# Optimization experiments

Measured on AMD Instinct MI355X. Metric: run time of the kernel, lower is better.

The kernel has to match this reference:

```python
import jax, jax.numpy as jnp
import numpy as np

B, C, H, W = 8, 256, 64, 64
HEADS = 8
DH = C // HEADS          # dim_head = in_ch // heads (as constructed in BasicTransBlock)
RS = 16                  # reduce_size
EPS = 1e-5               # BatchNorm eps


def _rel_pos_index():
    # Swin-style relative position index over the RS x RS reduced grid
    coords = np.stack(np.meshgrid(np.arange(RS), np.arange(RS), indexing='ij')).reshape(2, -1)
    rel = coords[:, :, None] - coords[:, None, :]
    rel = rel.transpose(1, 2, 0).copy()
    rel[:, :, 0] += RS - 1
    rel[:, :, 1] += RS - 1
    rel[:, :, 0] *= 2 * RS - 1
    return jnp.asarray(rel.sum(-1))  # [RS*RS, RS*RS] int

REL_IDX = _rel_pos_index()


def setup_inputs() -> dict:
    key = jax.random.key(0)
    ks = jax.random.split(key, 8)
    f32 = jnp.float32
    return {
        "x": jax.random.normal(ks[0], (B, C, H, W), f32),
        "bn1_gamma": jnp.ones((C,), f32),
        "bn1_beta": jnp.zeros((C,), f32),
        "bn1_mean": jnp.zeros((C,), f32),
        "bn1_var": jnp.ones((C,), f32),
        "qkv_dw": jax.random.normal(ks[1], (C, 1, 3, 3), f32) * 0.05,   # depthwise 3x3
        "qkv_pw": jax.random.normal(ks[2], (3 * C, C), f32) * 0.05,     # pointwise 1x1 -> 3C
        "out_dw": jax.random.normal(ks[3], (C, 1, 3, 3), f32) * 0.05,
        "out_pw": jax.random.normal(ks[4], (C, C), f32) * 0.05,
        "rel_table": jax.random.normal(ks[5], ((2 * RS - 1) ** 2, HEADS), f32) * 0.02,
        "bn2_gamma": jnp.ones((C,), f32),
        "bn2_beta": jnp.zeros((C,), f32),
        "bn2_mean": jnp.zeros((C,), f32),
        "bn2_var": jnp.ones((C,), f32),
        "mlp_w": jax.random.normal(ks[6], (C, C), f32) * 0.05,          # 1x1 conv, no bias
    }


def _bn(x, gamma, beta, mean, var):
    # inference-mode BatchNorm2d
    inv = gamma * jax.lax.rsqrt(var + EPS)
    return x * inv[None, :, None, None] + (beta - mean * inv)[None, :, None, None]


def _dwconv3(x, w):
    # depthwise 3x3, stride 1, padding 1
    return jax.lax.conv_general_dilated(
        x, w, (1, 1), 'SAME', feature_group_count=x.shape[1],
        dimension_numbers=('NCHW', 'OIHW', 'NCHW'))


def _interp_ac(x, oh, ow):
    # bilinear resize, align_corners=True (matches F.interpolate(..., align_corners=True))
    _, _, h, w = x.shape
    ys = jnp.linspace(0.0, h - 1.0, oh)
    xs = jnp.linspace(0.0, w - 1.0, ow)
    y0 = jnp.floor(ys).astype(jnp.int32); y1 = jnp.minimum(y0 + 1, h - 1)
    x0 = jnp.floor(xs).astype(jnp.int32); x1 = jnp.minimum(x0 + 1, w - 1)
    wy = (ys - y0.astype(ys.dtype))[:, None]   # [oh,1]
    wx = (xs - x0.astype(xs.dtype))            # [ow]
    v = x[:, :, y0, :] * (1 - wy) + x[:, :, y1, :] * wy      # [B,C,oh,w]
    return v[:, :, :, x0] * (1 - wx) + v[:, :, :, x1] * wx   # [B,C,oh,ow]


def _split_heads(t, h, w):
    # channel layout in rearrange is (dim_head heads): c = d*HEADS + head
    b = t.shape[0]
    return t.reshape(b, DH, HEADS, h * w).transpose(0, 2, 3, 1)  # [B,heads,hw,DH]


def _rel_bias(rel_table):
    bias = rel_table[REL_IDX.reshape(-1)].reshape(RS, RS, RS * RS, HEADS)
    bias = jnp.repeat(bias, H // RS, axis=0)   # expand rows to H
    bias = jnp.repeat(bias, W // RS, axis=1)   # expand cols to W
    return bias.reshape(H * W, RS * RS, HEADS).transpose(2, 0, 1)  # [heads, HW, RS*RS]


def reference(x, bn1_gamma, bn1_beta, bn1_mean, bn1_var,
              qkv_dw, qkv_pw, out_dw, out_pw, rel_table,
              bn2_gamma, bn2_beta, bn2_mean, bn2_var, mlp_w):
    out = _bn(x, bn1_gamma, bn1_beta, bn1_mean, bn1_var)

    # --- LinearAttention ---
    qkv = jnp.einsum('bchw,oc->bohw', _dwconv3(out, qkv_dw), qkv_pw)
    q, k, v = jnp.split(qkv, 3, axis=1)
    k = _interp_ac(k, RS, RS)
    v = _interp_ac(v, RS, RS)
    q = _split_heads(q, H, W)       # [B,heads,HW,DH]
    k = _split_heads(k, RS, RS)     # [B,heads,RS^2,DH]
    v = _split_heads(v, RS, RS)
    attn = jnp.einsum('bhid,bhjd->bhij', q, k)
    attn = (attn + _rel_bias(rel_table)[None]) * (DH ** -0.5)  # bias added BEFORE scale, as in source
    attn = jax.nn.softmax(attn, axis=-1)
    o = jnp.einsum('bhij,bhjd->bhid', attn, v)                 # [B,heads,HW,DH]
    o = o.transpose(0, 3, 1, 2).reshape(x.shape[0], C, H, W)   # inverse of (dim_head heads) split
    o = jnp.einsum('bchw,oc->bohw', _dwconv3(o, out_dw), out_pw)

    out = o + x
    residue = out
    out = jax.nn.relu(_bn(out, bn2_gamma, bn2_beta, bn2_mean, bn2_var))
    out = jnp.einsum('bchw,oc->bohw', out, mlp_w)
    return out + residue
```

## Files before the change

### kernel.cpp

```cpp
#include <hip/hip_runtime.h>
#include <hip/hip_bf16.h>
#include <math.h>

#define EPSF 1e-5f

typedef float f32x4 __attribute__((ext_vector_type(4)));
typedef short short8 __attribute__((ext_vector_type(8)));
typedef short short4v __attribute__((ext_vector_type(4)));
typedef unsigned short u16x4 __attribute__((ext_vector_type(4)));
typedef unsigned short u16x8 __attribute__((ext_vector_type(8)));

#if defined(__has_builtin)
#if __has_builtin(__builtin_amdgcn_mfma_f32_16x16x16bf16_1k)
#define HAVE_MFMA16 1
#endif
#endif
#ifndef HAVE_MFMA16
#define HAVE_MFMA16 0
#endif

static __device__ __forceinline__ unsigned short f2bf(float f) {
    unsigned u = __float_as_uint(f);
    u = (u + 0x7FFF + ((u >> 16) & 1)) >> 16;
    return (unsigned short)u;
}

static __device__ __forceinline__ float bf2f(unsigned short u) {
    return __uint_as_float((unsigned)u << 16);
}

static __device__ __forceinline__ unsigned packbf2(float a, float b) {
    __hip_bfloat162 t = __float22bfloat162_rn(float2{a, b});
    union { __hip_bfloat162 v; unsigned u; } cv;
    cv.v = t;
    return cv.u;
}

static __device__ __forceinline__ float fexp2(float x) {
    return __builtin_amdgcn_exp2f(x);
}

static __device__ __forceinline__ void lgkm_barrier() {
    asm volatile("s_waitcnt lgkmcnt(0)\n\ts_barrier" ::: "memory");
    __builtin_amdgcn_sched_barrier(0);
}

static __device__ __forceinline__ int swz(int r) { return ((r ^ (r >> 2)) & 7) << 1; }

#define ATTN_SCALE 0.17677669529663687f
#define LOG2E      1.4426950408889634f
#define QSCALE     (ATTN_SCALE * LOG2E)

template<bool BN, bool IB, bool OBF>
__global__ __launch_bounds__(256) void dwconv_k(
    const void* __restrict__ X, const float* __restrict__ DW,
    const float* __restrict__ g, const float* __restrict__ be,
    const float* __restrict__ mn, const float* __restrict__ vr,
    void* __restrict__ Out)
{
    int tid = threadIdx.x;
    int plane = blockIdx.x * 2 + (tid >> 7);
    int c = plane & 255;
    float inv = 1.f, ad = 0.f;
    if (BN) {
        inv = g[c] * rsqrtf(vr[c] + EPSF);
        ad  = be[c] - mn[c] * inv;
    }
    float w[9];
#pragma unroll
    for (int i = 0; i < 9; ++i) w[i] = DW[c * 9 + i];
    const float* Xf          = (const float*)X + (size_t)plane * 4096;
    const unsigned short* Xh = (const unsigned short*)X + (size_t)plane * 4096;
    int u  = tid & 127;
    int y0 = (u >> 3) * 4;
    int x0 = (u & 7) * 8;

    float r[6][16];
#pragma unroll
    for (int rr = 0; rr < 6; ++rr) {
        int yy = y0 + rr - 1;
        bool rv = (unsigned)yy < 64u;
#pragma unroll
        for (int gq = 0; gq < 4; ++gq) {
            int xx = x0 - 4 + gq * 4;
            f32x4 v = {0.f, 0.f, 0.f, 0.f};
            if (rv && (unsigned)xx < 64u) {
                if (IB) {
                    u16x4 u4 = *(const u16x4*)&Xh[yy * 64 + xx];
                    v[0] = bf2f(u4[0]); v[1] = bf2f(u4[1]);
                    v[2] = bf2f(u4[2]); v[3] = bf2f(u4[3]);
                } else {
                    v = *(const f32x4*)&Xf[yy * 64 + xx];
                }
                if (BN) {
#pragma unroll
                    for (int j = 0; j < 4; ++j) v[j] = v[j] * inv + ad;
                }
            }
            r[rr][gq * 4 + 0] = v[0]; r[rr][gq * 4 + 1] = v[1];
            r[rr][gq * 4 + 2] = v[2]; r[rr][gq * 4 + 3] = v[3];
        }
    }

#pragma unroll
    for (int j = 0; j < 4; ++j) {
        float acc[8] = {};
#pragma unroll
        for (int ky = 0; ky < 3; ++ky) {
#pragma unroll
            for (int kx = 0; kx < 3; ++kx) {
                float ww = w[ky * 3 + kx];
#pragma unroll
                for (int p = 0; p < 8; ++p)
                    acc[p] += ww * r[j + ky][3 + p + kx];
            }
        }
        if (OBF) {
            unsigned short* Ob = (unsigned short*)Out + (size_t)plane * 4096;
            int4 pk = { (int)packbf2(acc[0], acc[1]), (int)packbf2(acc[2], acc[3]),
                        (int)packbf2(acc[4], acc[5]), (int)packbf2(acc[6], acc[7]) };
            *(int4*)&Ob[(y0 + j) * 64 + x0] = pk;
        } else {
            float* Ob = (float*)Out + (size_t)plane * 4096;
            f32x4 lo = {acc[0], acc[1], acc[2], acc[3]};
            f32x4 hi = {acc[4], acc[5], acc[6], acc[7]};
            *(f32x4*)&Ob[(y0 + j) * 64 + x0]     = lo;
            *(f32x4*)&Ob[(y0 + j) * 64 + x0 + 4] = hi;
        }
    }
}

__global__ __launch_bounds__(256) void interp_k(
    const unsigned short* __restrict__ T, float* __restrict__ R)
{
    int bc = blockIdx.x;
    const unsigned short* Tb = T + (size_t)bc * 4096;
    int p  = threadIdx.x;
    int oy = p >> 4, ox = p & 15;
    const float st = 63.0f / 15.0f;
    float fy = oy * st, fx = ox * st;
    int y0 = (int)floorf(fy); int y1 = min(y0 + 1, 63); float wy = fy - (float)y0;
    int x0 = (int)floorf(fx); int x1 = min(x0 + 1, 63); float wx = fx - (float)x0;
    float v00 = bf2f(Tb[y0 * 64 + x0]), v01 = bf2f(Tb[y0 * 64 + x1]);
    float v10 = bf2f(Tb[y1 * 64 + x0]), v11 = bf2f(Tb[y1 * 64 + x1]);
    R[(size_t)bc * 256 + p] =
        (1.f - wy) * ((1.f - wx) * v00 + wx * v01) +
        wy         * ((1.f - wx) * v10 + wx * v11);
}

__global__ __launch_bounds__(256) void bias_k(
    const float* __restrict__ rel, float* __restrict__ btab)
{
    int idx = blockIdx.x * 256 + threadIdx.x;
    int h   = idx >> 16;
    int qc  = (idx >> 8) & 255;
    int key = idx & 255;
    int ay = qc >> 4, ax = qc & 15, by = key >> 4, bx = key & 15;
    int t = (ay - by + 15) * 31 + (ax - bx + 15);
    btab[idx] = rel[t * 8 + h] * QSCALE;
}

__global__ __launch_bounds__(256) void kvt_k(
    const unsigned short* __restrict__ kv,
    unsigned short* __restrict__ khat, unsigned short* __restrict__ vhat)
{
    __shared__ unsigned short kt_[32 * 260];
    int bh = blockIdx.x;
    int b = bh >> 3, h = bh & 7;
    const unsigned short* kvb = kv + (size_t)b * 512 * 256;
    int tid = threadIdx.x;

#pragma unroll
    for (int it = 0; it < 8; ++it) {
        int idx = it * 256 + tid;
        int d = idx >> 6, k4 = (idx & 63) * 4;
        ushort4 v = *(const ushort4*)&kvb[(size_t)(256 + d * 8 + h) * 256 + k4];
        *(ushort4*)&vhat[(size_t)bh * 8192 + d * 256 + k4] = v;
    }
#pragma unroll
    for (int it = 0; it < 8; ++it) {
        int idx = it * 256 + tid;
        int d = idx >> 6, k4 = (idx & 63) * 4;
        ushort4 v = *(const ushort4*)&kvb[(size_t)(d * 8 + h) * 256 + k4];
        *(ushort4*)&kt_[d * 260 + k4] = v;
    }
    __syncthreads();
#pragma unroll
    for (int it = 0; it < 8; ++it) {
        int idx = it * 256 + tid;
        int key = idx >> 3, dq = idx & 7;
        ushort4 o;
        o.x = kt_[(dq * 4 + 0) * 260 + key];
        o.y = kt_[(dq * 4 + 1) * 260 + key];
        o.z = kt_[(dq * 4 + 2) * 260 + key];
        o.w = kt_[(dq * 4 + 3) * 260 + key];
        *(ushort4*)&khat[(size_t)bh * 8192 + key * 32 + dq * 4] = o;
    }
}

template<int MODE, bool OB, bool AB, bool QHAT, bool XB>
__global__ __launch_bounds__(256) void mgemm_k(
    const void* __restrict__ A, const float* __restrict__ W,
    float* __restrict__ Out, const void* __restrict__ X,
    const float* __restrict__ g, const float* __restrict__ be,
    const float* __restrict__ mn, const float* __restrict__ vr,
    int M, int Ntot)
{
    __shared__ short Ws[128 * 256];
    __shared__ short As[128 * 64];
    int b = blockIdx.z, m0 = blockIdx.x * 128, n0 = blockIdx.y * 128;
    int tid = threadIdx.x;
    const float* Abf          = (const float*)A + (size_t)b * 256 * M;
    const unsigned short* Abh = (const unsigned short*)A + (size_t)b * 256 * M;

#pragma unroll
    for (int it = 0; it < 32; ++it) {
        int idx = it * 256 + tid;
        int n = idx >> 6, kq = idx & 63;
        f32x4 w4 = *(const f32x4*)&W[(size_t)(n0 + n) * 256 + kq * 4];
        short4v pk = { (short)f2bf(w4[0]), (short)f2bf(w4[1]),
                       (short)f2bf(w4[2]), (short)f2bf(w4[3]) };
        *(short4v*)&Ws[n * 256 + ((kq ^ swz(n)) << 2)] = pk;
    }

    constexpr bool RAW16 = AB && (MODE != 2);
    int mg = tid & 31, kg = tid >> 5;
    f32x4 rg[8];
    u16x4 rg16[8];
    auto load_tile = [&](int k0) {
#pragma unroll
        for (int half = 0; half < 2; ++half) {
#pragma unroll
            for (int i = 0; i < 4; ++i) {
                int c = k0 + kg * 4 + half * 32 + i;
                if (RAW16) {
                    rg16[half * 4 + i] = *(const u16x4*)&Abh[(size_t)c * M + m0 + mg * 4];
                } else if (AB) {
                    u16x4 r4 = *(const u16x4*)&Abh[(size_t)c * M + m0 + mg * 4];
                    float iv = g[c] * rsqrtf(vr[c] + EPSF);
                    float ad = be[c] - mn[c] * iv;
                    f32x4 v;
#pragma unroll
                    for (int j = 0; j < 4; ++j)
                        v[j] = fmaxf(bf2f(r4[j]) * iv + ad, 0.f);
                    rg[half * 4 + i] = v;
                } else {
                    f32x4 v = *(const f32x4*)&Abf[(size_t)c * M + m0 + mg * 4];
                    if (MODE == 2) {
                        float iv = g[c] * rsqrtf(vr[c] + EPSF);
                        float ad = be[c] - mn[c] * iv;
#pragma unroll
                        for (int j = 0; j < 4; ++j) v[j] = fmaxf(v[j] * iv + ad, 0.f);
                    }
                    rg[half * 4 + i] = v;
                }
            }
        }
    };
    load_tile(0);

    int w = tid >> 6, lane = tid & 63;
    int wm = w & 1, wn = w >> 1;
    int lg = lane >> 4, lc = lane & 15;
    f32x4 acc[4][4] = {};

    for (int k0 = 0; k0 < 256; k0 += 64) {
        __syncthreads();
#pragma unroll
        for (int half = 0; half < 2; ++half) {
#pragma unroll
            for (int j = 0; j < 4; ++j) {
                int m = mg * 4 + j;
                short4v pk;
                if (RAW16) {
                    pk = short4v{ (short)rg16[half * 4 + 0][j], (short)rg16[half * 4 + 1][j],
                                  (short)rg16[half * 4 + 2][j], (short)rg16[half * 4 + 3][j] };
                } else {
                    pk = short4v{ (short)f2bf(rg[half * 4 + 0][j]), (short)f2bf(rg[half * 4 + 1][j]),
                                  (short)f2bf(rg[half * 4 + 2][j]), (short)f2bf(rg[half * 4 + 3][j]) };
                }
                *(short4v*)&As[m * 64 + (((kg + half * 8) ^ swz(m)) << 2)] = pk;
            }
        }
        __syncthreads();
        if (k0 < 192) load_tile(k0 + 64);
#pragma unroll
        for (int ksl = 0; ksl < 2; ++ksl) {
            short8 wf[4], af[4];
            int gk = (k0 + ksl * 32 + lg * 8) >> 2;
            int ga = (ksl * 32 + lg * 8) >> 2;
#pragma unroll
            for (int nt = 0; nt < 4; ++nt) {
                int n = wn * 64 + nt * 16 + lc;
                wf[nt] = *(const short8*)&Ws[n * 256 + ((gk ^ swz(n)) << 2)];
            }
#pragma unroll
            for (int mt = 0; mt < 4; ++mt) {
                int m = wm * 64 + mt * 16 + lc;
                af[mt] = *(const short8*)&As[m * 64 + ((ga ^ swz(m)) << 2)];
            }
#pragma unroll
            for (int nt = 0; nt < 4; ++nt)
#pragma unroll
                for (int mt = 0; mt < 4; ++mt)
                    acc[nt][mt] = __builtin_amdgcn_mfma_f32_16x16x32_bf16(
                        wf[nt], af[mt], acc[nt][mt], 0, 0, 0);
        }
    }

    if (QHAT) {
        __syncthreads();
        unsigned short* Os = (unsigned short*)Ws;
#pragma unroll
        for (int nt = 0; nt < 4; ++nt)
#pragma unroll
            for (int mt = 0; mt < 4; ++mt)
#pragma unroll
                for (int reg = 0; reg < 4; ++reg) {
                    int nl = wn * 64 + nt * 16 + lg * 4 + reg;
                    int ml = wm * 64 + mt * 16 + lc;
                    Os[nl * 130 + ml] = f2bf(acc[nt][mt][reg] * QSCALE);
                }
        __syncthreads();
        unsigned short* Oq = (unsigned short*)Out;
        int dbase = n0 >> 3;
#pragma unroll
        for (int it = 0; it < 4; ++it) {
            int ri = it * 256 + tid;
            int hh = ri >> 7, ml = ri & 127;
            u16x8 lo, hi;
#pragma unroll
            for (int dd = 0; dd < 8; ++dd) {
                lo[dd] = Os[(dd * 8 + hh) * 130 + ml];
                hi[dd] = Os[((dd + 8) * 8 + hh) * 130 + ml];
            }
            size_t base = ((size_t)(b * 8 + hh) * 4096 + m0 + ml) * 32 + dbase;
            *(u16x8*)&Oq[base]     = lo;
            *(u16x8*)&Oq[base + 8] = hi;
        }
        return;
    }

    size_t ob = (size_t)b * Ntot * M;
#pragma unroll
    for (int nt = 0; nt < 4; ++nt) {
#pragma unroll
        for (int mt = 0; mt < 4; ++mt) {
#pragma unroll
            for (int reg = 0; reg < 4; ++reg) {
                int n = n0 + wn * 64 + nt * 16 + lg * 4 + reg;
                int m = m0 + wm * 64 + mt * 16 + lc;
                size_t addr = ob + (size_t)n * M + m;
                float v = acc[nt][mt][reg];
                if (MODE >= 1) {
                    float xv = XB ? bf2f(((const unsigned short*)X)[addr])
                                  : ((const float*)X)[addr];
                    v += xv;
                }
                if (OB) ((unsigned short*)Out)[addr] = f2bf(v);
                else    Out[addr] = v;
            }
        }
    }
}

__global__ __launch_bounds__(256) void attn_mfma_k(
    const unsigned short* __restrict__ Qh, const unsigned short* __restrict__ Khat,
    const unsigned short* __restrict__ Vhat,
    const float* __restrict__ btab, unsigned short* __restrict__ O)
{
    __shared__ float Om[2][4][16][36];
    __shared__ float Lw[2][4][16];

    int b = blockIdx.z, h = blockIdx.y, chunk = blockIdx.x;
    int tid = threadIdx.x;
    int w = tid >> 6, lane = tid & 63;
    int lg = lane >> 4, lc = lane & 15;
    int kw = w * 64;

    const unsigned short* Kb = Khat + (size_t)(b * 8 + h) * 8192;
    const unsigned short* Vb = Vhat + (size_t)(b * 8 + h) * 8192;
    const unsigned short* Qb = Qh + (size_t)(b * 8 + h) * 131072;
    unsigned short* Ob = O + (size_t)b * 256 * 4096;
    const float* bt = btab + (size_t)h * 65536;
    int rw = chunk * 128;

    int mrow = tid & 15, md = tid >> 4;

    short8 kf[4];
#pragma unroll
    for (int kt = 0; kt < 4; ++kt)
        kf[kt] = *(const short8*)&Kb[(kw + kt * 16 + lc) * 32 + lg * 8];

#if HAVE_MFMA16
    short4v vq[4][2];
#pragma unroll
    for (int kt = 0; kt < 4; ++kt) {
#pragma unroll
        for (int half = 0; half < 2; ++half)
            vq[kt][half] = *(const short4v*)&Vb[(half * 16 + lc) * 256 + kw + kt * 16 + lg * 4];
    }
#else
    int s1 = ((lg & 1) << 5) + lc;
    int s2 = s1 + 16;
    bool useOdd = (lg >> 1) != 0;
    short8 vf0[2], vf1[2];
#pragma unroll
    for (int ks = 0; ks < 2; ++ks) {
        vf0[ks] = *(const short8*)&Vb[lc * 256 + kw + ks * 32 + lg * 8];
        vf1[ks] = *(const short8*)&Vb[(16 + lc) * 256 + kw + ks * 32 + lg * 8];
    }
#endif

    auto compute = [&](int mt, int buf) {
        int rbase = rw + mt * 16;
        int r_a = rbase + lc;
        int qc = ((r_a >> 8) << 4) | ((r_a >> 2) & 15);
        const float* bq = bt + (size_t)qc * 256 + kw + lg * 4;

        f32x4 sacc[4];
#pragma unroll
        for (int kt = 0; kt < 4; ++kt)
            sacc[kt] = *(const f32x4*)&bq[kt * 16];

        short8 qf = *(const short8*)&Qb[(size_t)r_a * 32 + lg * 8];

#pragma unroll
        for (int kt = 0; kt < 4; ++kt)
            sacc[kt] = __builtin_amdgcn_mfma_f32_16x16x32_bf16(kf[kt], qf, sacc[kt], 0, 0, 0);

        float ls = 0.f;
        f32x4 o0 = {0.f, 0.f, 0.f, 0.f}, o1 = {0.f, 0.f, 0.f, 0.f};

#if HAVE_MFMA16
#pragma unroll
        for (int kt = 0; kt < 4; ++kt) {
            float p0 = fexp2(sacc[kt][0]);
            float p1 = fexp2(sacc[kt][1]);
            float p2 = fexp2(sacc[kt][2]);
            float p3 = fexp2(sacc[kt][3]);
            ls += (p0 + p1) + (p2 + p3);
            int2 pi = { (int)packbf2(p0, p1), (int)packbf2(p2, p3) };
            short4v pa = *(short4v*)&pi;
            o0 = __builtin_amdgcn_mfma_f32_16x16x16bf16_1k(pa, vq[kt][0], o0, 0, 0, 0);
            o1 = __builtin_amdgcn_mfma_f32_16x16x16bf16_1k(pa, vq[kt][1], o1, 0, 0, 0);
        }
        ls += __shfl_xor(ls, 16);
        ls += __shfl_xor(ls, 32);
#pragma unroll
        for (int reg = 0; reg < 4; ++reg) {
            Om[buf][w][lg * 4 + reg][lc]      = o0[reg];
            Om[buf][w][lg * 4 + reg][16 + lc] = o1[reg];
        }
#else
        unsigned plo[4], phi[4];
#pragma unroll
        for (int kt = 0; kt < 4; ++kt) {
            float p0 = fexp2(sacc[kt][0]);
            float p1 = fexp2(sacc[kt][1]);
            float p2 = fexp2(sacc[kt][2]);
            float p3 = fexp2(sacc[kt][3]);
            ls += (p0 + p1) + (p2 + p3);
            plo[kt] = packbf2(p0, p1);
            phi[kt] = packbf2(p2, p3);
        }
        ls += __shfl_xor(ls, 16);
        ls += __shfl_xor(ls, 32);
#pragma unroll
        for (int ks = 0; ks < 2; ++ks) {
            int eA = __shfl((int)plo[2 * ks], s1), oA = __shfl((int)plo[2 * ks + 1], s1);
            int eB = __shfl((int)phi[2 * ks], s1), oB = __shfl((int)phi[2 * ks + 1], s1);
            int eC = __shfl((int)plo[2 * ks], s2), oC = __shfl((int)plo[2 * ks + 1], s2);
            int eD = __shfl((int)phi[2 * ks], s2), oD = __shfl((int)phi[2 * ks + 1], s2);
            int4 pi = { useOdd ? oA : eA, useOdd ? oB : eB,
                        useOdd ? oC : eC, useOdd ? oD : eD };
            short8 pf = *(short8*)&pi;
            o0 = __builtin_amdgcn_mfma_f32_16x16x32_bf16(vf0[ks], pf, o0, 0, 0, 0);
            o1 = __builtin_amdgcn_mfma_f32_16x16x32_bf16(vf1[ks], pf, o1, 0, 0, 0);
        }
        *(f32x4*)&Om[buf][w][lc][lg * 4]      = o0;
        *(f32x4*)&Om[buf][w][lc][16 + lg * 4] = o1;
#endif
        if (lg == 0) Lw[buf][w][lc] = ls;
    };

    auto merge = [&](int mt, int buf) {
        int rbase = rw + mt * 16;
        float L = Lw[buf][0][mrow] + Lw[buf][1][mrow]
                + Lw[buf][2][mrow] + Lw[buf][3][mrow];
        float inv = __builtin_amdgcn_rcpf(L);
        float a0 = Om[buf][0][mrow][md] + Om[buf][1][mrow][md]
                 + Om[buf][2][mrow][md] + Om[buf][3][mrow][md];
        float a1 = Om[buf][0][mrow][md + 16] + Om[buf][1][mrow][md + 16]
                 + Om[buf][2][mrow][md + 16] + Om[buf][3][mrow][md + 16];
        unsigned pk = packbf2(a0 * inv, a1 * inv);
        Ob[(size_t)(md * 8 + h) * 4096 + rbase + mrow]        = (unsigned short)pk;
        Ob[(size_t)((md + 16) * 8 + h) * 4096 + rbase + mrow] = (unsigned short)(pk >> 16);
    };

    compute(0, 0);
    for (int mt = 0; mt < 8; ++mt) {
        lgkm_barrier();
        if (mt < 7) compute(mt + 1, (mt + 1) & 1);
        merge(mt, mt & 1);
    }
}

extern "C" void kernel_launch(void* const* d_in, const int* in_sizes, int n_in,
                              void* d_out, int out_size, void* d_ws, size_t ws_size,
                              hipStream_t stream)
{
    const float* x       = (const float*)d_in[0];
    const float* bn1_g   = (const float*)d_in[1];
    const float* bn1_b   = (const float*)d_in[2];
    const float* bn1_m   = (const float*)d_in[3];
    const float* bn1_v   = (const float*)d_in[4];
    const float* qkv_dw  = (const float*)d_in[5];
    const float* qkv_pw  = (const float*)d_in[6];
    const float* out_dw  = (const float*)d_in[7];
    const float* out_pw  = (const float*)d_in[8];
    const float* rel     = (const float*)d_in[9];
    const float* bn2_g   = (const float*)d_in[10];
    const float* bn2_b   = (const float*)d_in[11];
    const float* bn2_m   = (const float*)d_in[12];
    const float* bn2_v   = (const float*)d_in[13];
    const float* mlp_w   = (const float*)d_in[14];
    float* out = (float*)d_out;

    float* ws = (float*)d_ws;
    float* t    = ws;
    float* q    = ws + (size_t)8 * 1024 * 1024;
    float* tr   = ws + (size_t)16 * 1024 * 1024;
    float* kv   = tr + 524288;
    float* btab = kv + 524288;
    float* khat = btab + 524288;
    float* vhat = khat + 262144;
    float* o   = t;
    float* t2  = q;
    float* a   = t;

    bias_k<<<dim3(2048), 256, 0, stream>>>(rel, btab);

    dwconv_k<true, false, true><<<dim3(1024), 256, 0, stream>>>(
        x, qkv_dw, bn1_g, bn1_b, bn1_m, bn1_v, t);

    mgemm_k<0, true, true, true, false><<<dim3(32, 2, 8), 256, 0, stream>>>(
        t, qkv_pw, q, nullptr, nullptr, nullptr, nullptr, nullptr,
        4096, 256);

    interp_k<<<dim3(2048), 256, 0, stream>>>((const unsigned short*)t, tr);

    mgemm_k<0, true, false, false, false><<<dim3(2, 4, 8), 256, 0, stream>>>(
        tr, qkv_pw + 256 * 256, kv, nullptr, nullptr, nullptr, nullptr, nullptr,
        256, 512);

    kvt_k<<<dim3(64), 256, 0, stream>>>(
        (const unsigned short*)kv, (unsigned short*)khat, (unsigned short*)vhat);

    attn_mfma_k<<<dim3(32, 8, 8), 256, 0, stream>>>(
        (const unsigned short*)q, (const unsigned short*)khat,
        (const unsigned short*)vhat, btab, (unsigned short*)o);

    dwconv_k<false, true, true><<<dim3(1024), 256, 0, stream>>>(
        o, out_dw, nullptr, nullptr, nullptr, nullptr, t2);

    mgemm_k<1, true, true, false, false><<<dim3(32, 2, 8), 256, 0, stream>>>(
        t2, out_pw, (float*)a, x, nullptr, nullptr, nullptr, nullptr,
        4096, 256);

    mgemm_k<2, false, true, false, true><<<dim3(32, 2, 8), 256, 0, stream>>>(
        a, mlp_w, out, a, bn2_g, bn2_b, bn2_m, bn2_v,
        4096, 256);
}
```

Baseline: 129.3 us.

## Split attention work by query rows per wave instead of by key chunks

Each wave now owns 32 query rows and loops over all 256 keys itself, keeping the running sums in registers. Before, four waves split the keys and merged partial outputs through double-buffered shared memory with block barriers. This drops the cross-wave reduction, the barriers and most of the LDS traffic. In exchange every wave reloads the K/V fragments for each key chunk from global/L2 and holds more accumulator registers.

```diff
diff --git a/kernel.cpp b/kernel.cpp
--- a/kernel.cpp
+++ b/kernel.cpp
@@ -38,11 +38,6 @@
 
 static __device__ __forceinline__ float fexp2(float x) {
     return __builtin_amdgcn_exp2f(x);
-}
-
-static __device__ __forceinline__ void lgkm_barrier() {
-    asm volatile("s_waitcnt lgkmcnt(0)\n\ts_barrier" ::: "memory");
-    __builtin_amdgcn_sched_barrier(0);
 }
 
 static __device__ __forceinline__ int swz(int r) { return ((r ^ (r >> 2)) & 7) << 1; }
@@ -369,140 +364,143 @@
     const unsigned short* __restrict__ Vhat,
     const float* __restrict__ btab, unsigned short* __restrict__ O)
 {
-    __shared__ float Om[2][4][16][36];
-    __shared__ float Lw[2][4][16];
+    __shared__ float Ow[4][16][33];
 
     int b = blockIdx.z, h = blockIdx.y, chunk = blockIdx.x;
     int tid = threadIdx.x;
     int w = tid >> 6, lane = tid & 63;
     int lg = lane >> 4, lc = lane & 15;
-    int kw = w * 64;
 
     const unsigned short* Kb = Khat + (size_t)(b * 8 + h) * 8192;
     const unsigned short* Vb = Vhat + (size_t)(b * 8 + h) * 8192;
     const unsigned short* Qb = Qh + (size_t)(b * 8 + h) * 131072;
     unsigned short* Ob = O + (size_t)b * 256 * 4096;
     const float* bt = btab + (size_t)h * 65536;
-    int rw = chunk * 128;
-
-    int mrow = tid & 15, md = tid >> 4;
-
-    short8 kf[4];
-#pragma unroll
-    for (int kt = 0; kt < 4; ++kt)
-        kf[kt] = *(const short8*)&Kb[(kw + kt * 16 + lc) * 32 + lg * 8];
-
+    int rw = chunk * 128 + w * 32;
+
+    short8 qf[2];
+    int qc[2];
+#pragma unroll
+    for (int t = 0; t < 2; ++t) {
+        int r_a = rw + t * 16 + lc;
+        qf[t] = *(const short8*)&Qb[(size_t)r_a * 32 + lg * 8];
+        qc[t] = ((r_a >> 8) << 4) | ((r_a >> 2) & 15);
+    }
+
+    f32x4 o[2][2] = {};
+    float ls[2] = {0.f, 0.f};
+
+    for (int c = 0; c < 4; ++c) {
+        int kc = c * 64;
+        short8 kf[4];
+#pragma unroll
+        for (int kt = 0; kt < 4; ++kt)
+            kf[kt] = *(const short8*)&Kb[(kc + kt * 16 + lc) * 32 + lg * 8];
 #if HAVE_MFMA16
-    short4v vq[4][2];
-#pragma unroll
-    for (int kt = 0; kt < 4; ++kt) {
-#pragma unroll
-        for (int half = 0; half < 2; ++half)
-            vq[kt][half] = *(const short4v*)&Vb[(half * 16 + lc) * 256 + kw + kt * 16 + lg * 4];
-    }
+        short4v vq[4][2];
+#pragma unroll
+        for (int kt = 0; kt < 4; ++kt) {
+#pragma unroll
+            for (int half = 0; half < 2; ++half)
+                vq[kt][half] = *(const short4v*)&Vb[(half * 16 + lc) * 256 + kc + kt * 16 + lg * 4];
+        }
 #else
-    int s1 = ((lg & 1) << 5) + lc;
-    int s2 = s1 + 16;
-    bool useOdd = (lg >> 1) != 0;
-    short8 vf0[2], vf1[2];
-#pragma unroll
-    for (int ks = 0; ks < 2; ++ks) {
-        vf0[ks] = *(const short8*)&Vb[lc * 256 + kw + ks * 32 + lg * 8];
-        vf1[ks] = *(const short8*)&Vb[(16 + lc) * 256 + kw + ks * 32 + lg * 8];
-    }
-#endif
-
-    auto compute = [&](int mt, int buf) {
-        int rbase = rw + mt * 16;
-        int r_a = rbase + lc;
-        int qc = ((r_a >> 8) << 4) | ((r_a >> 2) & 15);
-        const float* bq = bt + (size_t)qc * 256 + kw + lg * 4;
-
-        f32x4 sacc[4];
-#pragma unroll
-        for (int kt = 0; kt < 4; ++kt)
-            sacc[kt] = *(const f32x4*)&bq[kt * 16];
-
-        short8 qf = *(const short8*)&Qb[(size_t)r_a * 32 + lg * 8];
-
-#pragma unroll
-        for (int kt = 0; kt < 4; ++kt)
-            sacc[kt] = __builtin_amdgcn_mfma_f32_16x16x32_bf16(kf[kt], qf, sacc[kt], 0, 0, 0);
-
-        float ls = 0.f;
-        f32x4 o0 = {0.f, 0.f, 0.f, 0.f}, o1 = {0.f, 0.f, 0.f, 0.f};
+        int s1 = ((lg & 1) << 5) + lc;
+        int s2 = s1 + 16;
+        bool useOdd = (lg >> 1) != 0;
+        short8 vf0[2], vf1[2];
+#pragma unroll
+        for (int ks = 0; ks < 2; ++ks) {
+            vf0[ks] = *(const short8*)&Vb[lc * 256 + kc + ks * 32 + lg * 8];
+            vf1[ks] = *(const short8*)&Vb[(16 + lc) * 256 + kc + ks * 32 + lg * 8];
+        }
+#endif
+
+#pragma unroll
+        for (int t = 0; t < 2; ++t) {
+            const float* bq = bt + (size_t)qc[t] * 256 + kc + lg * 4;
+            f32x4 sacc[4];
+#pragma unroll
+            for (int kt = 0; kt < 4; ++kt)
+                sacc[kt] = *(const f32x4*)&bq[kt * 16];
+#pragma unroll
+            for (int kt = 0; kt < 4; ++kt)
+                sacc[kt] = __builtin_amdgcn_mfma_f32_16x16x32_bf16(kf[kt], qf[t], sacc[kt], 0, 0, 0);
 
 #if HAVE_MFMA16
 #pragma unroll
-        for (int kt = 0; kt < 4; ++kt) {
-            float p0 = fexp2(sacc[kt][0]);
-            float p1 = fexp2(sacc[kt][1]);
-            float p2 = fexp2(sacc[kt][2]);
-            float p3 = fexp2(sacc[kt][3]);
-            ls += (p0 + p1) + (p2 + p3);
-            int2 pi = { (int)packbf2(p0, p1), (int)packbf2(p2, p3) };
-            short4v pa = *(short4v*)&pi;
-            o0 = __builtin_amdgcn_mfma_f32_16x16x16bf16_1k(pa, vq[kt][0], o0, 0, 0, 0);
-            o1 = __builtin_amdgcn_mfma_f32_16x16x16bf16_1k(pa, vq[kt][1], o1, 0, 0, 0);
-        }
-        ls += __shfl_xor(ls, 16);
-        ls += __shfl_xor(ls, 32);
+            for (int kt = 0; kt < 4; ++kt) {
+                float p0 = fexp2(sacc[kt][0]);
+                float p1 = fexp2(sacc[kt][1]);
+                float p2 = fexp2(sacc[kt][2]);
+                float p3 = fexp2(sacc[kt][3]);
+                ls[t] += (p0 + p1) + (p2 + p3);
+                int2 pi = { (int)packbf2(p0, p1), (int)packbf2(p2, p3) };
+                short4v pa = *(short4v*)&pi;
+                o[t][0] = __builtin_amdgcn_mfma_f32_16x16x16bf16_1k(pa, vq[kt][0], o[t][0], 0, 0, 0);
+                o[t][1] = __builtin_amdgcn_mfma_f32_16x16x16bf16_1k(pa, vq[kt][1], o[t][1], 0, 0, 0);
+            }
+#else
+            unsigned plo[4], phi[4];
+#pragma unroll
+            for (int kt = 0; kt < 4; ++kt) {
+                float p0 = fexp2(sacc[kt][0]);
+                float p1 = fexp2(sacc[kt][1]);
+                float p2 = fexp2(sacc[kt][2]);
+                float p3 = fexp2(sacc[kt][3]);
+                ls[t] += (p0 + p1) + (p2 + p3);
+                plo[kt] = packbf2(p0, p1);
+                phi[kt] = packbf2(p2, p3);
+            }
+#pragma unroll
+            for (int ks = 0; ks < 2; ++ks) {
+                int eA = __shfl((int)plo[2 * ks], s1), oA = __shfl((int)plo[2 * ks + 1], s1);
+                int eB = __shfl((int)phi[2 * ks], s1), oB = __shfl((int)phi[2 * ks + 1], s1);
+                int eC = __shfl((int)plo[2 * ks], s2), oC = __shfl((int)plo[2 * ks + 1], s2);
+                int eD = __shfl((int)phi[2 * ks], s2), oD = __shfl((int)phi[2 * ks + 1], s2);
+                int4 pi = { useOdd ? oA : eA, useOdd ? oB : eB,
+                            useOdd ? oC : eC, useOdd ? oD : eD };
+                short8 pf = *(short8*)&pi;
+                o[t][0] = __builtin_amdgcn_mfma_f32_16x16x32_bf16(vf0[ks], pf, o[t][0], 0, 0, 0);
+                o[t][1] = __builtin_amdgcn_mfma_f32_16x16x32_bf16(vf1[ks], pf, o[t][1], 0, 0, 0);
+            }
+#endif
+        }
+    }
+
+#pragma unroll
+    for (int t = 0; t < 2; ++t) {
+        float L = ls[t];
+        L += __shfl_xor(L, 16);
+        L += __shfl_xor(L, 32);
+        float inv = __builtin_amdgcn_rcpf(L);
+#if HAVE_MFMA16
 #pragma unroll
         for (int reg = 0; reg < 4; ++reg) {
-            Om[buf][w][lg * 4 + reg][lc]      = o0[reg];
-            Om[buf][w][lg * 4 + reg][16 + lc] = o1[reg];
+            Ow[w][lg * 4 + reg][lc]      = o[t][0][reg] * inv;
+            Ow[w][lg * 4 + reg][16 + lc] = o[t][1][reg] * inv;
         }
 #else
-        unsigned plo[4], phi[4];
-#pragma unroll
-        for (int kt = 0; kt < 4; ++kt) {
-            float p0 = fexp2(sacc[kt][0]);
-            float p1 = fexp2(sacc[kt][1]);
-            float p2 = fexp2(sacc[kt][2]);
-            float p3 = fexp2(sacc[kt][3]);
-            ls += (p0 + p1) + (p2 + p3);
-            plo[kt] = packbf2(p0, p1);
-            phi[kt] = packbf2(p2, p3);
-        }
-        ls += __shfl_xor(ls, 16);
-        ls += __shfl_xor(ls, 32);
-#pragma unroll
-        for (int ks = 0; ks < 2; ++ks) {
-            int eA = __shfl((int)plo[2 * ks], s1), oA = __shfl((int)plo[2 * ks + 1], s1);
-            int eB = __shfl((int)phi[2 * ks], s1), oB = __shfl((int)phi[2 * ks + 1], s1);
-            int eC = __shfl((int)plo[2 * ks], s2), oC = __shfl((int)plo[2 * ks + 1], s2);
-            int eD = __shfl((int)phi[2 * ks], s2), oD = __shfl((int)phi[2 * ks + 1], s2);
-            int4 pi = { useOdd ? oA : eA, useOdd ? oB : eB,
-                        useOdd ? oC : eC, useOdd ? oD : eD };
-            short8 pf = *(short8*)&pi;
-            o0 = __builtin_amdgcn_mfma_f32_16x16x32_bf16(vf0[ks], pf, o0, 0, 0, 0);
-            o1 = __builtin_amdgcn_mfma_f32_16x16x32_bf16(vf1[ks], pf, o1, 0, 0, 0);
-        }
-        *(f32x4*)&Om[buf][w][lc][lg * 4]      = o0;
-        *(f32x4*)&Om[buf][w][lc][16 + lg * 4] = o1;
-#endif
-        if (lg == 0) Lw[buf][w][lc] = ls;
-    };
-
-    auto merge = [&](int mt, int buf) {
-        int rbase = rw + mt * 16;
-        float L = Lw[buf][0][mrow] + Lw[buf][1][mrow]
-                + Lw[buf][2][mrow] + Lw[buf][3][mrow];
-        float inv = __builtin_amdgcn_rcpf(L);
-        float a0 = Om[buf][0][mrow][md] + Om[buf][1][mrow][md]
-                 + Om[buf][2][mrow][md] + Om[buf][3][mrow][md];
-        float a1 = Om[buf][0][mrow][md + 16] + Om[buf][1][mrow][md + 16]
-                 + Om[buf][2][mrow][md + 16] + Om[buf][3][mrow][md + 16];
-        unsigned pk = packbf2(a0 * inv, a1 * inv);
-        Ob[(size_t)(md * 8 + h) * 4096 + rbase + mrow]        = (unsigned short)pk;
-        Ob[(size_t)((md + 16) * 8 + h) * 4096 + rbase + mrow] = (unsigned short)(pk >> 16);
-    };
-
-    compute(0, 0);
-    for (int mt = 0; mt < 8; ++mt) {
-        lgkm_barrier();
-        if (mt < 7) compute(mt + 1, (mt + 1) & 1);
-        merge(mt, mt & 1);
+#pragma unroll
+        for (int reg = 0; reg < 4; ++reg) {
+            Ow[w][lc][lg * 4 + reg]      = o[t][0][reg] * inv;
+            Ow[w][lc][16 + lg * 4 + reg] = o[t][1][reg] * inv;
+        }
+#endif
+        asm volatile("s_waitcnt lgkmcnt(0)" ::: "memory");
+        int rbase = rw + t * 16;
+        int row = lane & 15, d0 = lane >> 4;
+#pragma unroll
+        for (int i = 0; i < 8; ++i) {
+            int d = d0 + 4 * i;
+#if HAVE_MFMA16
+            float v = Ow[w][row][d];
+#else
+            float v = Ow[w][row][d];
+#endif
+            Ob[(size_t)(d * 8 + h) * 4096 + rbase + row] = f2bf(v);
+        }
+        asm volatile("s_waitcnt lgkmcnt(0)" ::: "memory");
     }
 }
 
```

Result: slower. 145.2 us (+12.3%).
